# Optimization experiments

Measured on AMD Instinct MI355X. Metric: run time of the kernel, lower is better.

The kernel has to match this reference:

```python
import jax, jax.numpy as jnp
import numpy as np

N_EMBD = 1024
HEADS = 16
HEAD_DIM = N_EMBD // HEADS


def setup_inputs() -> dict:
    key = jax.random.key(0)
    k1, k2 = jax.random.split(key)
    x = jax.random.normal(k1, (2, 2048, N_EMBD), dtype=jnp.float32)
    W_qkv = jax.random.normal(k2, (N_EMBD, 3 * N_EMBD), dtype=jnp.float32) * (N_EMBD ** -0.5)
    b_qkv = jnp.zeros((3 * N_EMBD,), dtype=jnp.float32)
    return {"x": x, "W_qkv": W_qkv, "b_qkv": b_qkv}


def reference(x, W_qkv, b_qkv):
    B, T, _ = x.shape
    qkv = x @ W_qkv + b_qkv                      # [B, T, 3*n_embd]
    q, k, v = jnp.split(qkv, 3, axis=-1)
    q = q.reshape(B, T, HEADS, HEAD_DIM)
    k = k.reshape(B, T, HEADS, HEAD_DIM)
    v = v.reshape(B, T, HEADS, HEAD_DIM)
    attn = jnp.einsum('bthd,bThd->bhtT', q, k) / jnp.sqrt(jnp.float32(HEAD_DIM))
    causal = jnp.tril(jnp.ones((T, T), dtype=bool))  # [T, T]
    attn = jnp.where(causal, attn, -jnp.inf)
    attn = jax.nn.softmax(attn, axis=-1)
    # dropout is identity in deterministic/eval mode (training=False)
    out = jnp.einsum('bhtT,bThd->bthd', attn, v).reshape(B, T, N_EMBD)
    return out
```

## Files before the change

### kernel.cpp

```cpp
#include <hip/hip_runtime.h>
#include <hip/hip_bf16.h>

#define BATCH 2
#define TSEQ  2048
#define NEMBD 1024
#define HEADS 16
#define HDIM  64

typedef short          bf16x8 __attribute__((ext_vector_type(8)));
typedef float          f32x4  __attribute__((ext_vector_type(4)));
typedef unsigned short u16;

__device__ __forceinline__ u16 f2bf(float f) {
  unsigned int u = __float_as_uint(f);
  u += 0x7fffu + ((u >> 16) & 1u);
  return (u16)(u >> 16);
}

__device__ __forceinline__ void gld16(const u16* g, u16* l) {
  __builtin_amdgcn_global_load_lds(
      (const __attribute__((address_space(1))) unsigned int*)g,
      (__attribute__((address_space(3))) unsigned int*)l, 16, 0, 0);
}

__global__ __launch_bounds__(256) void k_convert_x(const float* __restrict__ x,
                                                   u16* __restrict__ xb) {
  int i = blockIdx.x * 256 + threadIdx.x;
  float4 v = ((const float4*)x)[i];
  ushort4 o;
  o.x = f2bf(v.x); o.y = f2bf(v.y); o.z = f2bf(v.z); o.w = f2bf(v.w);
  ((ushort4*)xb)[i] = o;
}

__global__ __launch_bounds__(256) void k_transpose_w(const float* __restrict__ w,
                                                     u16* __restrict__ wt) {
  __shared__ float tile[32][33];
  const int n0 = blockIdx.x * 32;
  const int k0 = blockIdx.y * 32;
  const int t  = threadIdx.x;
  const int r  = t >> 3;
  const int c4 = (t & 7) * 4;
  float4 v = *(const float4*)(w + (size_t)(k0 + r) * 3072 + n0 + c4);
  tile[r][c4 + 0] = v.x; tile[r][c4 + 1] = v.y;
  tile[r][c4 + 2] = v.z; tile[r][c4 + 3] = v.w;
  __syncthreads();
  ushort4 o;
  o.x = f2bf(tile[c4 + 0][r]);
  o.y = f2bf(tile[c4 + 1][r]);
  o.z = f2bf(tile[c4 + 2][r]);
  o.w = f2bf(tile[c4 + 3][r]);
  *(ushort4*)(wt + (size_t)(n0 + r) * 1024 + k0 + c4) = o;
}

__global__ __launch_bounds__(256, 3) void k_qkv_gemm(
    const u16* __restrict__ xb, const u16* __restrict__ wt,
    const float* __restrict__ bias,
    u16* __restrict__ qb, u16* __restrict__ kbuf, u16* __restrict__ vt) {
  __shared__ __align__(16) u16 As[128 * 64];
  __shared__ __align__(16) u16 Bs[128 * 64];

  const int t    = threadIdx.x;
  const int wv   = t >> 6;
  const int lane = t & 63;
  const int m    = lane & 15;
  const int quad = lane >> 4;
  const int lin  = blockIdx.x;
  const int cp   = lin >> 5;
  const int rp   = ((lin & 7) << 2) | ((lin >> 3) & 3);
  const int row0 = rp * 128;
  const int col0 = cp * 128;
  const int wr   = (wv >> 1) * 64;
  const int wc   = (wv & 1) * 64;

  const int sr = wv * 32 + (lane >> 3);
  const int gs = (lane & 7) ^ (sr & 7);
  const u16* ag = xb + (size_t)(row0 + sr) * 1024 + gs * 8;
  const u16* bg = wt + (size_t)(col0 + sr) * 1024 + gs * 8;
  u16* al = As + (wv * 32) * 64;
  u16* bl = Bs + (wv * 32) * 64;

  f32x4 acc[4][4];
  const f32x4 zf = {0.f, 0.f, 0.f, 0.f};
  for (int i = 0; i < 4; ++i)
    for (int j = 0; j < 4; ++j) acc[i][j] = zf;

  for (int kt = 0; kt < 16; ++kt) {
    const int kk = kt * 64;
    __syncthreads();
    gld16(ag + kk,             al);
    gld16(ag + kk +  8 * 1024, al +  8 * 64);
    gld16(ag + kk + 16 * 1024, al + 16 * 64);
    gld16(ag + kk + 24 * 1024, al + 24 * 64);
    gld16(bg + kk,             bl);
    gld16(bg + kk +  8 * 1024, bl +  8 * 64);
    gld16(bg + kk + 16 * 1024, bl + 16 * 64);
    gld16(bg + kk + 24 * 1024, bl + 24 * 64);
    __syncthreads();

#pragma unroll
    for (int h = 0; h < 2; ++h) {
      const int g = ((quad + 4 * h) ^ (m & 7)) * 8;
      bf16x8 af[4], bfr[4];
#pragma unroll
      for (int mt = 0; mt < 4; ++mt)
        af[mt] = *(const bf16x8*)(As + (wr + mt * 16 + m) * 64 + g);
#pragma unroll
      for (int nt = 0; nt < 4; ++nt)
        bfr[nt] = *(const bf16x8*)(Bs + (wc + nt * 16 + m) * 64 + g);
#pragma unroll
      for (int mt = 0; mt < 4; ++mt)
#pragma unroll
        for (int nt = 0; nt < 4; ++nt)
          acc[mt][nt] = __builtin_amdgcn_mfma_f32_16x16x32_bf16(
              af[mt], bfr[nt], acc[mt][nt], 0, 0, 0);
    }
  }

  const int sec = col0 >> 10;
#pragma unroll
  for (int nt = 0; nt < 4; ++nt) {
    const int Cc = col0 + wc + nt * 16 + m;
    const float bv = bias[Cc];
    const int c = Cc & 1023;
    const int h = c >> 6;
    const int d = c & 63;
#pragma unroll
    for (int mt = 0; mt < 4; ++mt) {
      const int Rbase = row0 + wr + mt * 16 + quad * 4;
      const int bb = Rbase >> 11;
      const int t0 = Rbase & 2047;
      const int bh = bb * HEADS + h;
      if (sec == 0) {
#pragma unroll
        for (int rg = 0; rg < 4; ++rg) {
          float v = (acc[mt][nt][rg] + bv) * 0.125f;
          qb[(size_t)(bh * TSEQ + t0 + rg) * HDIM + d] = f2bf(v);
        }
      } else if (sec == 1) {
#pragma unroll
        for (int rg = 0; rg < 4; ++rg) {
          float v = acc[mt][nt][rg] + bv;
          kbuf[(size_t)(bh * TSEQ + t0 + rg) * HDIM + d] = f2bf(v);
        }
      } else {
        ushort4 pk;
        pk.x = f2bf(acc[mt][nt][0] + bv);
        pk.y = f2bf(acc[mt][nt][1] + bv);
        pk.z = f2bf(acc[mt][nt][2] + bv);
        pk.w = f2bf(acc[mt][nt][3] + bv);
        *(ushort4*)(vt + (size_t)(bh * HDIM + d) * TSEQ + t0) = pk;
      }
    }
  }
}

__global__ __launch_bounds__(256, 3) void k_attn(
    const u16* __restrict__ qb, const u16* __restrict__ kbuf,
    const u16* __restrict__ vt, float* __restrict__ out) {
  __shared__ __align__(16) u16 Kb[2][4096];
  __shared__ __align__(16) u16 Vb[2][4096];
  __shared__ __align__(16) u16 pt[4][16 * 72];

  const int t     = threadIdx.x;
  const int wv    = t >> 6;
  const int lane  = t & 63;
  const int m     = lane & 15;
  const int quad  = lane >> 4;
  const int bh    = blockIdx.x & 31;
  const int qtg   = 31 - (blockIdx.x >> 5);
  const int qbase = (qtg * 4 + wv) * 16;
  const int nkt   = qtg + 1;

  u16* pw = &pt[wv][0];

  const u16* qrow = qb + ((size_t)bh * TSEQ + qbase + m) * HDIM + quad * 8;
  bf16x8 aq0 = *(const bf16x8*)(qrow);
  bf16x8 aq1 = *(const bf16x8*)(qrow + 32);

  const int sr = wv * 16 + (lane >> 3);
  const int gs = (lane & 7) ^ (sr & 7);
  const u16* kg = kbuf + ((size_t)bh * TSEQ + sr) * HDIM + gs * 8;
  const u16* vg = vt + ((size_t)bh * HDIM + sr) * TSEQ + gs * 8;
  u16* klds = &Kb[0][wv * 16 * 64];
  u16* vlds = &Vb[0][wv * 16 * 64];

  const int swL = (quad ^ (m & 7)) * 8;
  const int swH = ((quad + 4) ^ (m & 7)) * 8;

  f32x4 o[4];
  const f32x4 zf = {0.f, 0.f, 0.f, 0.f};
  for (int nt = 0; nt < 4; ++nt) o[nt] = zf;
  float rsum = 0.f;
  const int qi = qbase + m;

  gld16(kg,             klds);
  gld16(kg + 8 * HDIM,  klds + 8 * 64);
  gld16(vg,             vlds);
  gld16(vg + 8 * TSEQ,  vlds + 8 * 64);
  __syncthreads();

  for (int kt = 0; kt < nkt; ++kt) {
    const int b = kt & 1;
    const u16* kb0 = &Kb[b][0];
    const u16* vb0 = &Vb[b][0];

    f32x4 s[4];
    for (int nt = 0; nt < 4; ++nt) s[nt] = zf;
#pragma unroll
    for (int nt = 0; nt < 4; ++nt) {
      bf16x8 kf = *(const bf16x8*)(kb0 + (nt * 16 + m) * 64 + swL);
      s[nt] = __builtin_amdgcn_mfma_f32_16x16x32_bf16(kf, aq0, s[nt], 0, 0, 0);
    }
#pragma unroll
    for (int nt = 0; nt < 4; ++nt) {
      bf16x8 kf = *(const bf16x8*)(kb0 + (nt * 16 + m) * 64 + swH);
      s[nt] = __builtin_amdgcn_mfma_f32_16x16x32_bf16(kf, aq1, s[nt], 0, 0, 0);
    }

    bf16x8 vfL[4], vfH[4];
#pragma unroll
    for (int nt = 0; nt < 4; ++nt) {
      vfL[nt] = *(const bf16x8*)(vb0 + (nt * 16 + m) * 64 + swL);
      vfH[nt] = *(const bf16x8*)(vb0 + (nt * 16 + m) * 64 + swH);
    }

    if (kt + 1 < nkt) {
      const int nb = (kt + 1) & 1;
      const u16* kgn = kg + (size_t)(kt + 1) * 64 * HDIM;
      const u16* vgn = vg + (kt + 1) * 64;
      u16* kl = &Kb[nb][wv * 16 * 64];
      u16* vl = &Vb[nb][wv * 16 * 64];
      gld16(kgn,            kl);
      gld16(kgn + 8 * HDIM, kl + 8 * 64);
      gld16(vgn,            vl);
      gld16(vgn + 8 * TSEQ, vl + 8 * 64);
    }

    if (kt == nkt - 1) {
      const int kb = kt * 64 + quad * 4;
#pragma unroll
      for (int nt = 0; nt < 4; ++nt)
#pragma unroll
        for (int rg = 0; rg < 4; ++rg)
          if (kb + nt * 16 + rg > qi) s[nt][rg] = -1e30f;
    }

#pragma unroll
    for (int nt = 0; nt < 4; ++nt) {
      float p0 = __expf(s[nt][0]), p1 = __expf(s[nt][1]);
      float p2 = __expf(s[nt][2]), p3 = __expf(s[nt][3]);
      rsum += (p0 + p1) + (p2 + p3);
      ushort4 pk = {f2bf(p0), f2bf(p1), f2bf(p2), f2bf(p3)};
      *(ushort4*)(pw + m * 72 + nt * 16 + quad * 4) = pk;
    }
    bf16x8 bp0 = *(const bf16x8*)(pw + m * 72 + quad * 8);
    bf16x8 bp1 = *(const bf16x8*)(pw + m * 72 + 32 + quad * 8);

#pragma unroll
    for (int nt = 0; nt < 4; ++nt)
      o[nt] = __builtin_amdgcn_mfma_f32_16x16x32_bf16(vfL[nt], bp0, o[nt], 0, 0, 0);
#pragma unroll
    for (int nt = 0; nt < 4; ++nt)
      o[nt] = __builtin_amdgcn_mfma_f32_16x16x32_bf16(vfH[nt], bp1, o[nt], 0, 0, 0);

    __syncthreads();
  }

  rsum += __shfl_xor(rsum, 16);
  rsum += __shfl_xor(rsum, 32);
  const float inv = 1.0f / rsum;

  const int bb = bh >> 4;
  const int h  = bh & 15;
  float* ob = out + ((size_t)(bb * TSEQ + qi) * NEMBD + h * HDIM + quad * 4);
#pragma unroll
  for (int nt = 0; nt < 4; ++nt) {
    float4 st;
    st.x = o[nt][0] * inv; st.y = o[nt][1] * inv;
    st.z = o[nt][2] * inv; st.w = o[nt][3] * inv;
    *(float4*)(ob + nt * 16) = st;
  }
}

extern "C" void kernel_launch(void* const* d_in, const int* in_sizes, int n_in,
                              void* d_out, int out_size, void* d_ws, size_t ws_size,
                              hipStream_t stream) {
  (void)in_sizes; (void)n_in; (void)out_size; (void)ws_size;
  const float* x    = (const float*)d_in[0];
  const float* W    = (const float*)d_in[1];
  const float* bqkv = (const float*)d_in[2];
  float* out = (float*)d_out;

  u16* ws   = (u16*)d_ws;
  u16* qb   = ws;
  u16* kbuf = ws + 4194304;
  u16* vt   = ws + 2 * 4194304;
  u16* xb   = ws + 3 * 4194304;
  u16* wt   = ws + 4 * 4194304;

  hipLaunchKernelGGL(k_convert_x, dim3(4096), dim3(256), 0, stream, x, xb);
  hipLaunchKernelGGL(k_transpose_w, dim3(96, 32), dim3(256), 0, stream, W, wt);
  hipLaunchKernelGGL(k_qkv_gemm, dim3(768), dim3(256), 0, stream,
                     xb, wt, bqkv, qb, kbuf, vt);
  hipLaunchKernelGGL(k_attn, dim3(1024), dim3(256), 0, stream,
                     qb, kbuf, vt, out);
}
```

Measured before the change: 139.6 us.

## Process two 16-row query groups per wave to double K/V tile reuse

Each wave now handles 32 query rows as two 16-row groups, so every block covers 128 query rows and the grid is halved. Each K/V tile loaded into LDS feeds twice as many MFMAs. Waves skip compute on K tiles beyond their causal diagonal, which leaves some waves idle near the diagonal. Softmax and PV for the second group are interleaved with the first to overlap exp work with MFMAs. The cost is higher register pressure under launch_bounds(256,3), fewer blocks for load balancing, and more intra-block imbalance.

```diff
diff --git a/kernel.cpp b/kernel.cpp
--- a/kernel.cpp
+++ b/kernel.cpp
@@ -159,7 +159,7 @@
     const u16* __restrict__ vt, float* __restrict__ out) {
   __shared__ __align__(16) u16 Kb[2][4096];
   __shared__ __align__(16) u16 Vb[2][4096];
-  __shared__ __align__(16) u16 pt[4][16 * 72];
+  __shared__ __align__(16) u16 pt[4][2 * 1152];
 
   const int t     = threadIdx.x;
   const int wv    = t >> 6;
@@ -167,15 +167,20 @@
   const int m     = lane & 15;
   const int quad  = lane >> 4;
   const int bh    = blockIdx.x & 31;
-  const int qtg   = 31 - (blockIdx.x >> 5);
-  const int qbase = (qtg * 4 + wv) * 16;
-  const int nkt   = qtg + 1;
-
-  u16* pw = &pt[wv][0];
-
-  const u16* qrow = qb + ((size_t)bh * TSEQ + qbase + m) * HDIM + quad * 8;
-  bf16x8 aq0 = *(const bf16x8*)(qrow);
-  bf16x8 aq1 = *(const bf16x8*)(qrow + 32);
+  const int qtg   = 15 - (blockIdx.x >> 5);
+  const int qbase = (qtg * 4 + wv) * 32;
+  const int nkt   = 2 * qtg + 2;
+  const int maskTile = qbase >> 6;
+
+  u16* pw0 = &pt[wv][0];
+  u16* pw1 = &pt[wv][1152];
+
+  const u16* qrow0 = qb + ((size_t)bh * TSEQ + qbase + m) * HDIM + quad * 8;
+  const u16* qrow1 = qrow0 + 16 * HDIM;
+  bf16x8 aq0g0 = *(const bf16x8*)(qrow0);
+  bf16x8 aq1g0 = *(const bf16x8*)(qrow0 + 32);
+  bf16x8 aq0g1 = *(const bf16x8*)(qrow1);
+  bf16x8 aq1g1 = *(const bf16x8*)(qrow1 + 32);
 
   const int sr = wv * 16 + (lane >> 3);
   const int gs = (lane & 7) ^ (sr & 7);
@@ -187,11 +192,12 @@
   const int swL = (quad ^ (m & 7)) * 8;
   const int swH = ((quad + 4) ^ (m & 7)) * 8;
 
-  f32x4 o[4];
+  f32x4 o0[4], o1[4];
   const f32x4 zf = {0.f, 0.f, 0.f, 0.f};
-  for (int nt = 0; nt < 4; ++nt) o[nt] = zf;
-  float rsum = 0.f;
-  const int qi = qbase + m;
+  for (int nt = 0; nt < 4; ++nt) { o0[nt] = zf; o1[nt] = zf; }
+  float rsum0 = 0.f, rsum1 = 0.f;
+  const int qi0 = qbase + m;
+  const int qi1 = qbase + 16 + m;
 
   gld16(kg,             klds);
   gld16(kg + 8 * HDIM,  klds + 8 * 64);
@@ -203,25 +209,52 @@
     const int b = kt & 1;
     const u16* kb0 = &Kb[b][0];
     const u16* vb0 = &Vb[b][0];
-
-    f32x4 s[4];
-    for (int nt = 0; nt < 4; ++nt) s[nt] = zf;
-#pragma unroll
-    for (int nt = 0; nt < 4; ++nt) {
-      bf16x8 kf = *(const bf16x8*)(kb0 + (nt * 16 + m) * 64 + swL);
-      s[nt] = __builtin_amdgcn_mfma_f32_16x16x32_bf16(kf, aq0, s[nt], 0, 0, 0);
-    }
-#pragma unroll
-    for (int nt = 0; nt < 4; ++nt) {
-      bf16x8 kf = *(const bf16x8*)(kb0 + (nt * 16 + m) * 64 + swH);
-      s[nt] = __builtin_amdgcn_mfma_f32_16x16x32_bf16(kf, aq1, s[nt], 0, 0, 0);
-    }
+    const bool active = (kt <= maskTile);
 
     bf16x8 vfL[4], vfH[4];
-#pragma unroll
-    for (int nt = 0; nt < 4; ++nt) {
-      vfL[nt] = *(const bf16x8*)(vb0 + (nt * 16 + m) * 64 + swL);
-      vfH[nt] = *(const bf16x8*)(vb0 + (nt * 16 + m) * 64 + swH);
+    f32x4 s0[4], s1[4];
+
+    if (active) {
+      for (int nt = 0; nt < 4; ++nt) { s0[nt] = zf; s1[nt] = zf; }
+#pragma unroll
+      for (int nt = 0; nt < 4; ++nt) {
+        bf16x8 kf = *(const bf16x8*)(kb0 + (nt * 16 + m) * 64 + swL);
+        s0[nt] = __builtin_amdgcn_mfma_f32_16x16x32_bf16(kf, aq0g0, s0[nt], 0, 0, 0);
+        s1[nt] = __builtin_amdgcn_mfma_f32_16x16x32_bf16(kf, aq0g1, s1[nt], 0, 0, 0);
+      }
+#pragma unroll
+      for (int nt = 0; nt < 4; ++nt) {
+        bf16x8 kf = *(const bf16x8*)(kb0 + (nt * 16 + m) * 64 + swH);
+        s0[nt] = __builtin_amdgcn_mfma_f32_16x16x32_bf16(kf, aq1g0, s0[nt], 0, 0, 0);
+        s1[nt] = __builtin_amdgcn_mfma_f32_16x16x32_bf16(kf, aq1g1, s1[nt], 0, 0, 0);
+      }
+
+      if (kt == maskTile) {
+        const int kb_ = kt * 64 + quad * 4;
+#pragma unroll
+        for (int nt = 0; nt < 4; ++nt)
+#pragma unroll
+          for (int rg = 0; rg < 4; ++rg) {
+            const int kj = kb_ + nt * 16 + rg;
+            if (kj > qi0) s0[nt][rg] = -1e30f;
+            if (kj > qi1) s1[nt][rg] = -1e30f;
+          }
+      }
+
+#pragma unroll
+      for (int nt = 0; nt < 4; ++nt) {
+        float p0 = __expf(s0[nt][0]), p1 = __expf(s0[nt][1]);
+        float p2 = __expf(s0[nt][2]), p3 = __expf(s0[nt][3]);
+        rsum0 += (p0 + p1) + (p2 + p3);
+        ushort4 pk = {f2bf(p0), f2bf(p1), f2bf(p2), f2bf(p3)};
+        *(ushort4*)(pw0 + m * 72 + nt * 16 + quad * 4) = pk;
+      }
+
+#pragma unroll
+      for (int nt = 0; nt < 4; ++nt) {
+        vfL[nt] = *(const bf16x8*)(vb0 + (nt * 16 + m) * 64 + swL);
+        vfH[nt] = *(const bf16x8*)(vb0 + (nt * 16 + m) * 64 + swH);
+      }
     }
 
     if (kt + 1 < nkt) {
@@ -236,49 +269,58 @@
       gld16(vgn + 8 * TSEQ, vl + 8 * 64);
     }
 
-    if (kt == nkt - 1) {
-      const int kb = kt * 64 + quad * 4;
-#pragma unroll
-      for (int nt = 0; nt < 4; ++nt)
-#pragma unroll
-        for (int rg = 0; rg < 4; ++rg)
-          if (kb + nt * 16 + rg > qi) s[nt][rg] = -1e30f;
-    }
-
-#pragma unroll
-    for (int nt = 0; nt < 4; ++nt) {
-      float p0 = __expf(s[nt][0]), p1 = __expf(s[nt][1]);
-      float p2 = __expf(s[nt][2]), p3 = __expf(s[nt][3]);
-      rsum += (p0 + p1) + (p2 + p3);
-      ushort4 pk = {f2bf(p0), f2bf(p1), f2bf(p2), f2bf(p3)};
-      *(ushort4*)(pw + m * 72 + nt * 16 + quad * 4) = pk;
-    }
-    bf16x8 bp0 = *(const bf16x8*)(pw + m * 72 + quad * 8);
-    bf16x8 bp1 = *(const bf16x8*)(pw + m * 72 + 32 + quad * 8);
-
-#pragma unroll
-    for (int nt = 0; nt < 4; ++nt)
-      o[nt] = __builtin_amdgcn_mfma_f32_16x16x32_bf16(vfL[nt], bp0, o[nt], 0, 0, 0);
-#pragma unroll
-    for (int nt = 0; nt < 4; ++nt)
-      o[nt] = __builtin_amdgcn_mfma_f32_16x16x32_bf16(vfH[nt], bp1, o[nt], 0, 0, 0);
+    if (active) {
+      bf16x8 bp00 = *(const bf16x8*)(pw0 + m * 72 + quad * 8);
+      bf16x8 bp01 = *(const bf16x8*)(pw0 + m * 72 + 32 + quad * 8);
+#pragma unroll
+      for (int nt = 0; nt < 4; ++nt)
+        o0[nt] = __builtin_amdgcn_mfma_f32_16x16x32_bf16(vfL[nt], bp00, o0[nt], 0, 0, 0);
+#pragma unroll
+      for (int nt = 0; nt < 4; ++nt)
+        o0[nt] = __builtin_amdgcn_mfma_f32_16x16x32_bf16(vfH[nt], bp01, o0[nt], 0, 0, 0);
+
+#pragma unroll
+      for (int nt = 0; nt < 4; ++nt) {
+        float p0 = __expf(s1[nt][0]), p1 = __expf(s1[nt][1]);
+        float p2 = __expf(s1[nt][2]), p3 = __expf(s1[nt][3]);
+        rsum1 += (p0 + p1) + (p2 + p3);
+        ushort4 pk = {f2bf(p0), f2bf(p1), f2bf(p2), f2bf(p3)};
+        *(ushort4*)(pw1 + m * 72 + nt * 16 + quad * 4) = pk;
+      }
+      bf16x8 bp10 = *(const bf16x8*)(pw1 + m * 72 + quad * 8);
+      bf16x8 bp11 = *(const bf16x8*)(pw1 + m * 72 + 32 + quad * 8);
+#pragma unroll
+      for (int nt = 0; nt < 4; ++nt)
+        o1[nt] = __builtin_amdgcn_mfma_f32_16x16x32_bf16(vfL[nt], bp10, o1[nt], 0, 0, 0);
+#pragma unroll
+      for (int nt = 0; nt < 4; ++nt)
+        o1[nt] = __builtin_amdgcn_mfma_f32_16x16x32_bf16(vfH[nt], bp11, o1[nt], 0, 0, 0);
+    }
 
     __syncthreads();
   }
 
-  rsum += __shfl_xor(rsum, 16);
-  rsum += __shfl_xor(rsum, 32);
-  const float inv = 1.0f / rsum;
+  rsum0 += __shfl_xor(rsum0, 16);
+  rsum0 += __shfl_xor(rsum0, 32);
+  rsum1 += __shfl_xor(rsum1, 16);
+  rsum1 += __shfl_xor(rsum1, 32);
+  const float inv0 = 1.0f / rsum0;
+  const float inv1 = 1.0f / rsum1;
 
   const int bb = bh >> 4;
   const int h  = bh & 15;
-  float* ob = out + ((size_t)(bb * TSEQ + qi) * NEMBD + h * HDIM + quad * 4);
+  float* ob0 = out + ((size_t)(bb * TSEQ + qi0) * NEMBD + h * HDIM + quad * 4);
+  float* ob1 = out + ((size_t)(bb * TSEQ + qi1) * NEMBD + h * HDIM + quad * 4);
 #pragma unroll
   for (int nt = 0; nt < 4; ++nt) {
     float4 st;
-    st.x = o[nt][0] * inv; st.y = o[nt][1] * inv;
-    st.z = o[nt][2] * inv; st.w = o[nt][3] * inv;
-    *(float4*)(ob + nt * 16) = st;
+    st.x = o0[nt][0] * inv0; st.y = o0[nt][1] * inv0;
+    st.z = o0[nt][2] * inv0; st.w = o0[nt][3] * inv0;
+    *(float4*)(ob0 + nt * 16) = st;
+    float4 su;
+    su.x = o1[nt][0] * inv1; su.y = o1[nt][1] * inv1;
+    su.z = o1[nt][2] * inv1; su.w = o1[nt][3] * inv1;
+    *(float4*)(ob1 + nt * 16) = su;
   }
 }
 
@@ -302,6 +344,6 @@
   hipLaunchKernelGGL(k_transpose_w, dim3(96, 32), dim3(256), 0, stream, W, wt);
   hipLaunchKernelGGL(k_qkv_gemm, dim3(768), dim3(256), 0, stream,
                      xb, wt, bqkv, qb, kbuf, vt);
-  hipLaunchKernelGGL(k_attn, dim3(1024), dim3(256), 0, stream,
+  hipLaunchKernelGGL(k_attn, dim3(512), dim3(256), 0, stream,
                      qb, kbuf, vt, out);
 }
```

Result: slower. 149.7 us (+7.2%).
